# Kernel tuning notes

Measured on AMD Instinct MI355X. Metric: run time of the kernel, lower is better.

Reference implementation:

```python
import jax, jax.numpy as jnp
import numpy as np

B, S, D, H = 4, 2048, 1024, 16
DEPTH = D // H  # 64


def setup_inputs() -> dict:
    key = jax.random.key(0)
    ks = jax.random.split(key, 11)
    scale = 1.0 / np.sqrt(D)
    inp = {
        "v": jax.random.normal(ks[0], (B, S, D), jnp.float32),
        "k": jax.random.normal(ks[1], (B, S, D), jnp.float32),
        "q": jax.random.normal(ks[2], (B, S, D), jnp.float32),
        # causal mask: 1.0 where attention is disallowed (strict upper triangle)
        "mask": jnp.triu(jnp.ones((S, S), jnp.float32), k=1)[None, None, :, :],
        "wq": jax.random.normal(ks[3], (D, D), jnp.float32) * scale,
        "bq": jnp.zeros((D,), jnp.float32),
        "wk": jax.random.normal(ks[4], (D, D), jnp.float32) * scale,
        "bk": jnp.zeros((D,), jnp.float32),
        "wv": jax.random.normal(ks[5], (D, D), jnp.float32) * scale,
        "bv": jnp.zeros((D,), jnp.float32),
        "wo": jax.random.normal(ks[6], (D, D), jnp.float32) * scale,
        "bo": jnp.zeros((D,), jnp.float32),
    }
    return inp


def _split_heads(x):
    # [B, S, D] -> [B, H, S, depth]
    b, s, _ = x.shape
    return x.reshape(b, s, H, DEPTH).transpose(0, 2, 1, 3)


def reference(v, k, q, mask, wq, bq, wk, bk, wv, bv, wo, bo):
    qh = _split_heads(q @ wq + bq)  # [B,H,S,depth]
    kh = _split_heads(k @ wk + bk)
    vh = _split_heads(v @ wv + bv)

    logits = jnp.einsum("bhqd,bhkd->bhqk", qh, kh) / jnp.sqrt(
        jnp.asarray(DEPTH, jnp.float32)
    )
    logits = logits + mask * -1e9
    attn = jax.nn.softmax(logits, axis=-1)  # [B,H,S,S]
    out = jnp.einsum("bhqk,bhkd->bhqd", attn, vh)
    out = out.transpose(0, 2, 1, 3).reshape(q.shape[0], -1, D)  # [B,S,D]
    return out @ wo + bo
```

## Files before the change

### kernel.cpp

```cpp
#include <hip/hip_runtime.h>

typedef _Float16 f16;
typedef _Float16 half8 __attribute__((ext_vector_type(8)));
typedef _Float16 half4v __attribute__((ext_vector_type(4)));
typedef _Float16 half2v __attribute__((ext_vector_type(2)));
typedef float f32x4 __attribute__((ext_vector_type(4)));

__device__ __forceinline__ void gl_lds16(const void* g, void* l) {
    __builtin_amdgcn_global_load_lds((const __attribute__((address_space(1))) void*)g,
                                     (__attribute__((address_space(3))) void*)l, 16, 0, 0);
}

__device__ __forceinline__ unsigned pack_f16(float a, float b) {
    union { half2v h; unsigned u; } un;
    un.h[0] = (f16)a; un.h[1] = (f16)b;
    return un.u;
}

__global__ __launch_bounds__(256) void cvt_f32_f16(const float* __restrict__ x, f16* __restrict__ y)
{
    const size_t i = ((size_t)blockIdx.x * 256 + threadIdx.x) * 8;
    const float4 a = *(const float4*)(x + i);
    const float4 b = *(const float4*)(x + i + 4);
    half8 h;
    h[0] = (f16)a.x; h[1] = (f16)a.y; h[2] = (f16)a.z; h[3] = (f16)a.w;
    h[4] = (f16)b.x; h[5] = (f16)b.y; h[6] = (f16)b.z; h[7] = (f16)b.w;
    *(half8*)(y + i) = h;
}

__device__ __forceinline__ void prep_w_body(const float* __restrict__ W, f16* __restrict__ Wt)
{
    __shared__ float t[64][65];
    const int tid = threadIdx.x;
    const int tk = blockIdx.x * 64, tn = blockIdx.y * 64;
    const int rr = tid >> 4, cc = (tid & 15) * 4;
    #pragma unroll
    for (int j = 0; j < 4; ++j) {
        float4 v = *(const float4*)(W + (size_t)(tk + rr + j * 16) * 1024 + tn + cc);
        t[rr + j * 16][cc] = v.x; t[rr + j * 16][cc + 1] = v.y;
        t[rr + j * 16][cc + 2] = v.z; t[rr + j * 16][cc + 3] = v.w;
    }
    __syncthreads();
    const int n = tid >> 2, kc = (tid & 3) * 16;
    f16 o[16];
    #pragma unroll
    for (int j = 0; j < 16; ++j) o[j] = (f16)t[kc + j][n];
    f16* dst = Wt + (size_t)(tn + n) * 1024 + tk + kc;
    *(uint4*)dst = *(uint4*)o;
    *(uint4*)(dst + 8) = *(uint4*)(o + 8);
}

__global__ __launch_bounds__(256) void prep_w1(const float* __restrict__ W, f16* __restrict__ Wt)
{ prep_w_body(W, Wt); }

__global__ __launch_bounds__(256) void prep_w3(const float* __restrict__ w0,
    const float* __restrict__ w1, const float* __restrict__ w2, f16* __restrict__ Wt)
{
    const int z = blockIdx.z;
    const float* W = (z == 0) ? w0 : (z == 1) ? w1 : w2;
    prep_w_body(W, Wt + (size_t)z * 1024 * 1024);
}

template<int OUT>
__global__ __launch_bounds__(256, 2) void gemm_kernel(
    const f16* __restrict__ X, const f16* __restrict__ Wt,
    const float* __restrict__ bias, void* __restrict__ outv)
{
    __shared__ __align__(16) f16 As[2][128 * 64];
    __shared__ __align__(16) f16 Bs[2][128 * 64];

    const int tid = threadIdx.x;
    const int lane = tid & 63;
    const int lane16 = lane & 15, quad = lane >> 4;
    const int wave = tid >> 6;
    const int wm = (wave >> 1) * 64, wn = (wave & 1) * 64;

    const int lin = blockIdx.x + 8 * blockIdx.y;
    const int xcd = lin & 7, t = lin >> 3;
    const int m0 = ((t >> 3) * 8 + xcd) * 128;
    const int n0 = (t & 7) * 128;

    const int wbase = tid & 192;
    const int srow = tid >> 3, schunk = tid & 7;

    f32x4 acc[4][4] = {};

    #pragma unroll
    for (int i = 0; i < 4; ++i) {
        const int row = i * 32 + srow;
        const int sw = (schunk ^ (row & 7)) * 8;
        gl_lds16(Wt + (size_t)(n0 + row) * 1024 + sw, Bs[0] + (size_t)(i * 256 + wbase) * 8);
        gl_lds16(X  + (size_t)(m0 + row) * 1024 + sw, As[0] + (size_t)(i * 256 + wbase) * 8);
    }

    for (int kt = 0; kt < 16; ++kt) {
        if (kt + 1 < 16) {
            const int nb = (kt + 1) & 1;
            const int k1 = (kt + 1) * 64;
            #pragma unroll
            for (int i = 0; i < 4; ++i) {
                const int row = i * 32 + srow;
                const int sw = (schunk ^ (row & 7)) * 8;
                gl_lds16(Wt + (size_t)(n0 + row) * 1024 + k1 + sw, Bs[nb] + (size_t)(i * 256 + wbase) * 8);
                gl_lds16(X  + (size_t)(m0 + row) * 1024 + k1 + sw, As[nb] + (size_t)(i * 256 + wbase) * 8);
            }
            asm volatile("s_waitcnt vmcnt(8)" ::: "memory");
        } else {
            asm volatile("s_waitcnt vmcnt(0)" ::: "memory");
        }
        __builtin_amdgcn_s_barrier();
        asm volatile("" ::: "memory");

        const f16* Ab = As[kt & 1];
        const f16* Bb = Bs[kt & 1];
        half8 af[4][2], bf[4][2];
        #pragma unroll
        for (int i = 0; i < 4; ++i) {
            const int ra = wm + i * 16 + lane16;
            const int rb = wn + i * 16 + lane16;
            #pragma unroll
            for (int c = 0; c < 2; ++c) {
                af[i][c] = *(const half8*)(Ab + ra * 64 + (((c * 4 + quad) ^ (ra & 7)) * 8));
                bf[i][c] = *(const half8*)(Bb + rb * 64 + (((c * 4 + quad) ^ (rb & 7)) * 8));
            }
        }
        #pragma unroll
        for (int c = 0; c < 2; ++c)
            #pragma unroll
            for (int mi = 0; mi < 4; ++mi)
                #pragma unroll
                for (int ni = 0; ni < 4; ++ni)
                    acc[mi][ni] = __builtin_amdgcn_mfma_f32_16x16x32_f16(af[mi][c], bf[ni][c], acc[mi][ni], 0, 0, 0);

        asm volatile("" ::: "memory");
        __builtin_amdgcn_s_barrier();
        asm volatile("" ::: "memory");
    }

    #pragma unroll
    for (int mi = 0; mi < 4; ++mi) {
        #pragma unroll
        for (int ni = 0; ni < 4; ++ni) {
            const int col = n0 + wn + ni * 16 + lane16;
            const float bval = bias[col];
            const int grow0 = m0 + wm + mi * 16 + quad * 4;
            if (OUT == 2) {
                const int b = grow0 >> 11, s0 = grow0 & 2047;
                const int h = col >> 6, d = col & 63;
                half4v p;
                #pragma unroll
                for (int r = 0; r < 4; ++r) p[r] = (f16)(acc[mi][ni][r] + bval);
                *(half4v*)((f16*)outv + (((size_t)b * 16 + h) * 64 + d) * 2048 + s0) = p;
            } else if (OUT == 0) {
                #pragma unroll
                for (int r = 0; r < 4; ++r)
                    ((f16*)outv)[(size_t)(grow0 + r) * 1024 + col] = (f16)(acc[mi][ni][r] + bval);
            } else {
                #pragma unroll
                for (int r = 0; r < 4; ++r)
                    ((float*)outv)[(size_t)(grow0 + r) * 1024 + col] = acc[mi][ni][r] + bval;
            }
        }
    }
}

__global__ __launch_bounds__(256, 4) void attn_kernel(
    const f16* __restrict__ qh, const f16* __restrict__ kh,
    const f16* __restrict__ vt, f16* __restrict__ at)
{
    __shared__ __align__(16) f16 Ks[2][64 * 64];
    __shared__ __align__(16) f16 Vts[2][64 * 64];

    const int tid = threadIdx.x;
    const int lane = tid & 63, wave = tid >> 6;
    const int lane16 = lane & 15, quad = lane >> 4;
    const int wbase = tid & 192;
    const int l3 = lane16 & 7;
    const int srow = tid >> 3, schunk = tid & 7;

    const int lin = blockIdx.x + 16 * blockIdx.y;
    const int xcd = lin & 7, t = lin >> 3;
    const int bh = xcd + 8 * (t & 7);
    const int qi = 15 - (t >> 3);
    const int b = bh >> 4, h = bh & 15;

    const f16* qp = qh + (size_t)b * 2048 * 1024 + h * 64;
    const f16* kp = kh + (size_t)b * 2048 * 1024 + h * 64;
    const f16* vtp = vt + (size_t)bh * 64 * 2048;

    const int qb = 128 * qi;
    const int qrow0 = qb + wave * 32;
    const int ntiles = qb / 64 + 2;
    const int qmax = qrow0 + 31;

    #pragma unroll
    for (int i = 0; i < 2; ++i) {
        const int row = i * 32 + srow;
        const int sw = (schunk ^ (row & 7)) * 8;
        gl_lds16(kp + (size_t)row * 1024 + sw, Ks[0] + (size_t)(i * 256 + wbase) * 8);
        gl_lds16(vtp + (size_t)row * 2048 + sw, Vts[0] + (size_t)(i * 256 + wbase) * 8);
    }

    half8 aq[2][2];
    #pragma unroll
    for (int mt = 0; mt < 2; ++mt)
        #pragma unroll
        for (int c = 0; c < 2; ++c)
            aq[mt][c] = *(const half8*)(qp + (size_t)(qrow0 + mt * 16 + lane16) * 1024 + c * 32 + quad * 8);

    f32x4 o[4][2] = {};
    float lp[2] = {0.0f, 0.0f};

    for (int kt = 0; kt < ntiles; ++kt) {
        if (kt + 1 < ntiles) {
            const int nb = (kt + 1) & 1;
            const int k1 = (kt + 1) * 64;
            #pragma unroll
            for (int i = 0; i < 2; ++i) {
                const int row = i * 32 + srow;
                const int sw = (schunk ^ (row & 7)) * 8;
                gl_lds16(kp + (size_t)(k1 + row) * 1024 + sw, Ks[nb] + (size_t)(i * 256 + wbase) * 8);
                gl_lds16(vtp + (size_t)row * 2048 + k1 + sw, Vts[nb] + (size_t)(i * 256 + wbase) * 8);
            }
            asm volatile("s_waitcnt vmcnt(4)" ::: "memory");
        } else {
            asm volatile("s_waitcnt vmcnt(0)" ::: "memory");
        }
        __builtin_amdgcn_s_barrier();
        asm volatile("" ::: "memory");

        const int k0 = kt * 64;
        if (k0 <= qmax) {
            const f16* Kb = Ks[kt & 1];
            const f16* Vb = Vts[kt & 1];
            f32x4 sT[4][2];
            #pragma unroll
            for (int sub = 0; sub < 4; ++sub) {
                const int kr = sub * 16 + lane16;
                const half8 ak0 = *(const half8*)(Kb + kr * 64 + ((quad ^ l3) * 8));
                const half8 ak1 = *(const half8*)(Kb + kr * 64 + (((4 + quad) ^ l3) * 8));
                #pragma unroll
                for (int mt = 0; mt < 2; ++mt) {
                    f32x4 z = {};
                    z = __builtin_amdgcn_mfma_f32_16x16x32_f16(ak0, aq[mt][0], z, 0, 0, 0);
                    z = __builtin_amdgcn_mfma_f32_16x16x32_f16(ak1, aq[mt][1], z, 0, 0, 0);
                    sT[sub][mt] = z;
                }
            }
            const bool needmask = (k0 + 63 > qrow0);
            if (needmask) {
                #pragma unroll
                for (int sub = 0; sub < 4; ++sub)
                    #pragma unroll
                    for (int mt = 0; mt < 2; ++mt)
                        #pragma unroll
                        for (int r = 0; r < 4; ++r) {
                            const int key = k0 + sub * 16 + quad * 4 + r;
                            const int qi2 = qrow0 + mt * 16 + lane16;
                            if (key > qi2) sT[sub][mt][r] = -1e30f;
                        }
            }

            half8 bp[2][2];
            #pragma unroll
            for (int mt = 0; mt < 2; ++mt) {
                unsigned pk01[4], pk23[4];
                #pragma unroll
                for (int sub = 0; sub < 4; ++sub) {
                    float p[4];
                    #pragma unroll
                    for (int r = 0; r < 4; ++r) {
                        const float x = fmaf(sT[sub][mt][r], 0.18033688011112042f, -5.770780163555852f);
                        float e;
                        asm("v_exp_f32 %0, %1" : "=v"(e) : "v"(x));
                        p[r] = e;
                        lp[mt] += e;
                    }
                    pk01[sub] = pack_f16(p[0], p[1]);
                    pk23[sub] = pack_f16(p[2], p[3]);
                }
                #pragma unroll
                for (int c = 0; c < 2; ++c) {
                    unsigned a0 = pk01[2 * c], b0 = pk01[2 * c + 1];
                    unsigned a1 = pk23[2 * c], b1 = pk23[2 * c + 1];
                    asm("v_permlane32_swap_b32 %0, %1" : "+v"(a0), "+v"(b0));
                    asm("v_permlane16_swap_b32 %0, %1" : "+v"(a0), "+v"(b0));
                    asm("v_permlane32_swap_b32 %0, %1" : "+v"(a1), "+v"(b1));
                    asm("v_permlane16_swap_b32 %0, %1" : "+v"(a1), "+v"(b1));
                    union { unsigned u[4]; half8 h8; } un;
                    un.u[0] = a0; un.u[1] = a1; un.u[2] = b0; un.u[3] = b1;
                    bp[c][mt] = un.h8;
                }
            }

            #pragma unroll
            for (int nt = 0; nt < 4; ++nt) {
                const int dr = nt * 16 + lane16;
                const half8 av0 = *(const half8*)(Vb + dr * 64 + ((quad ^ l3) * 8));
                const half8 av1 = *(const half8*)(Vb + dr * 64 + (((4 + quad) ^ l3) * 8));
                #pragma unroll
                for (int mt = 0; mt < 2; ++mt) {
                    o[nt][mt] = __builtin_amdgcn_mfma_f32_16x16x32_f16(av0, bp[0][mt], o[nt][mt], 0, 0, 0);
                    o[nt][mt] = __builtin_amdgcn_mfma_f32_16x16x32_f16(av1, bp[1][mt], o[nt][mt], 0, 0, 0);
                }
            }
        }
        asm volatile("" ::: "memory");
        __builtin_amdgcn_s_barrier();
        asm volatile("" ::: "memory");
    }

    #pragma unroll
    for (int mt = 0; mt < 2; ++mt) {
        float red = lp[mt];
        red += __shfl_xor(red, 16);
        red += __shfl_xor(red, 32);
        const float inv = 1.0f / red;
        const int sr = qrow0 + mt * 16 + lane16;
        f16* dst = at + ((size_t)b * 2048 + sr) * 1024 + h * 64 + quad * 4;
        #pragma unroll
        for (int nt = 0; nt < 4; ++nt) {
            half4v p;
            #pragma unroll
            for (int r = 0; r < 4; ++r) p[r] = (f16)(o[nt][mt][r] * inv);
            *(half4v*)(dst + nt * 16) = p;
        }
    }
}

extern "C" void kernel_launch(void* const* d_in, const int* in_sizes, int n_in,
                              void* d_out, int out_size, void* d_ws, size_t ws_size,
                              hipStream_t stream)
{
    const float* v  = (const float*)d_in[0];
    const float* k  = (const float*)d_in[1];
    const float* q  = (const float*)d_in[2];
    const float* wq = (const float*)d_in[4];
    const float* bq = (const float*)d_in[5];
    const float* wk = (const float*)d_in[6];
    const float* bk = (const float*)d_in[7];
    const float* wv = (const float*)d_in[8];
    const float* bv = (const float*)d_in[9];
    const float* wo = (const float*)d_in[10];
    const float* bo = (const float*)d_in[11];

    f16* qh = (f16*)d_ws;
    f16* kh = qh + (size_t)8 * 1024 * 1024;
    f16* vt = kh + (size_t)8 * 1024 * 1024;
    f16* at = vt + (size_t)8 * 1024 * 1024;

    f16* wT = (f16*)d_out;
    f16* wqT = wT;
    f16* wkT = wT + (size_t)1024 * 1024;
    f16* wvT = wT + (size_t)2 * 1024 * 1024;
    f16* xf  = wT + (size_t)3 * 1024 * 1024;
    f16* woT = qh;

    prep_w3<<<dim3(16, 16, 3), 256, 0, stream>>>(wq, wk, wv, wT);

    dim3 g(8, 64);
    cvt_f32_f16<<<4096, 256, 0, stream>>>(q, xf);
    gemm_kernel<0><<<g, 256, 0, stream>>>(xf, wqT, bq, qh);
    cvt_f32_f16<<<4096, 256, 0, stream>>>(k, xf);
    gemm_kernel<0><<<g, 256, 0, stream>>>(xf, wkT, bk, kh);
    cvt_f32_f16<<<4096, 256, 0, stream>>>(v, xf);
    gemm_kernel<2><<<g, 256, 0, stream>>>(xf, wvT, bv, vt);

    attn_kernel<<<dim3(16, 64), 256, 0, stream>>>(qh, kh, vt, at);

    prep_w1<<<dim3(16, 16), 256, 0, stream>>>(wo, woT);
    gemm_kernel<1><<<g, 256, 0, stream>>>(at, woT, bo, d_out);
}
```

Measured before the change: 313.3 us.

## Fuse fp32-to-fp16 input conversion into a single batched QKV GEMM launch

Removes the three standalone fp32→fp16 conversion kernels. The QKV projection GEMM now loads fp32 activations straight into registers, converts them, and writes them to LDS during the pipelined K loop. The three projection GEMMs are also merged into one launch with a z-dimension of three, which cuts launch count and gives a larger grid. The cost is that A-tile loads go through registers instead of async global-to-LDS copies, which adds register pressure and a conversion step inside the main loop.

```diff
diff --git a/kernel.cpp b/kernel.cpp
--- a/kernel.cpp
+++ b/kernel.cpp
@@ -17,17 +17,6 @@
     return un.u;
 }
 
-__global__ __launch_bounds__(256) void cvt_f32_f16(const float* __restrict__ x, f16* __restrict__ y)
-{
-    const size_t i = ((size_t)blockIdx.x * 256 + threadIdx.x) * 8;
-    const float4 a = *(const float4*)(x + i);
-    const float4 b = *(const float4*)(x + i + 4);
-    half8 h;
-    h[0] = (f16)a.x; h[1] = (f16)a.y; h[2] = (f16)a.z; h[3] = (f16)a.w;
-    h[4] = (f16)b.x; h[5] = (f16)b.y; h[6] = (f16)b.z; h[7] = (f16)b.w;
-    *(half8*)(y + i) = h;
-}
-
 __device__ __forceinline__ void prep_w_body(const float* __restrict__ W, f16* __restrict__ Wt)
 {
     __shared__ float t[64][65];
@@ -61,13 +50,19 @@
     prep_w_body(W, Wt + (size_t)z * 1024 * 1024);
 }
 
-template<int OUT>
-__global__ __launch_bounds__(256, 2) void gemm_kernel(
-    const f16* __restrict__ X, const f16* __restrict__ Wt,
-    const float* __restrict__ bias, void* __restrict__ outv)
+__global__ __launch_bounds__(256, 2) void qkv_gemm(
+    const float* __restrict__ Xq, const float* __restrict__ Xk, const float* __restrict__ Xv,
+    const f16* __restrict__ Wt,
+    const float* __restrict__ bqp, const float* __restrict__ bkp, const float* __restrict__ bvp,
+    f16* __restrict__ qh, f16* __restrict__ kh, f16* __restrict__ vth)
 {
     __shared__ __align__(16) f16 As[2][128 * 64];
-    __shared__ __align__(16) f16 Bs[2][128 * 64];
+    __shared__ __align__(16) f16 Ws[2][128 * 64];
+
+    const int z = blockIdx.z;
+    const float* X    = (z == 0) ? Xq : (z == 1) ? Xk : Xv;
+    const float* bias = (z == 0) ? bqp : (z == 1) ? bkp : bvp;
+    const f16*   W    = Wt + (size_t)z * 1024 * 1024;
 
     const int tid = threadIdx.x;
     const int lane = tid & 63;
@@ -81,16 +76,150 @@
     const int n0 = (t & 7) * 128;
 
     const int wbase = tid & 192;
+    const int srow = tid >> 3;
+    const int sch  = tid & 7;
+    const int swc  = sch ^ (srow & 7);
+
+    const size_t xgbase = (size_t)(m0 + srow) * 1024 + sch * 8;
+    const size_t wgbase = (size_t)(n0 + srow) * 1024 + swc * 8;
+    f16* const pA0 = As[0] + srow * 64 + swc * 8;
+    f16* const pA1 = As[1] + srow * 64 + swc * 8;
+
+    f32x4 acc[4][4] = {};
+
+    {
+        float4 xr[4][2];
+        #pragma unroll
+        for (int i = 0; i < 4; ++i) {
+            xr[i][0] = *(const float4*)(X + xgbase + (size_t)i * 32768);
+            xr[i][1] = *(const float4*)(X + xgbase + (size_t)i * 32768 + 4);
+        }
+        #pragma unroll
+        for (int i = 0; i < 4; ++i)
+            gl_lds16(W + wgbase + (size_t)i * 32768, Ws[0] + (size_t)(i * 256 + wbase) * 8);
+        asm volatile("s_waitcnt vmcnt(4)" ::: "memory");
+        #pragma unroll
+        for (int i = 0; i < 4; ++i) {
+            half8 hx;
+            hx[0] = (f16)xr[i][0].x; hx[1] = (f16)xr[i][0].y;
+            hx[2] = (f16)xr[i][0].z; hx[3] = (f16)xr[i][0].w;
+            hx[4] = (f16)xr[i][1].x; hx[5] = (f16)xr[i][1].y;
+            hx[6] = (f16)xr[i][1].z; hx[7] = (f16)xr[i][1].w;
+            *(half8*)(pA0 + i * 2048) = hx;
+        }
+        asm volatile("s_waitcnt vmcnt(0) lgkmcnt(0)" ::: "memory");
+        __builtin_amdgcn_s_barrier();
+        asm volatile("" ::: "memory");
+    }
+
+    for (int kt = 0; kt < 16; ++kt) {
+        const int cur = kt & 1, nb = cur ^ 1;
+        float4 xr[4][2];
+        if (kt + 1 < 16) {
+            const int k1 = (kt + 1) * 64;
+            const float* xs = X + xgbase + k1;
+            #pragma unroll
+            for (int i = 0; i < 4; ++i) {
+                xr[i][0] = *(const float4*)(xs + (size_t)i * 32768);
+                xr[i][1] = *(const float4*)(xs + (size_t)i * 32768 + 4);
+            }
+            const f16* ws = W + wgbase + k1;
+            #pragma unroll
+            for (int i = 0; i < 4; ++i)
+                gl_lds16(ws + (size_t)i * 32768, Ws[nb] + (size_t)(i * 256 + wbase) * 8);
+        }
+
+        const f16* Ab = As[cur];
+        const f16* Bb = Ws[cur];
+        half8 af[4][2], bf[4][2];
+        #pragma unroll
+        for (int i = 0; i < 4; ++i) {
+            const int ra = wm + i * 16 + lane16;
+            const int rb = wn + i * 16 + lane16;
+            #pragma unroll
+            for (int c = 0; c < 2; ++c) {
+                af[i][c] = *(const half8*)(Ab + ra * 64 + (((c * 4 + quad) ^ (ra & 7)) * 8));
+                bf[i][c] = *(const half8*)(Bb + rb * 64 + (((c * 4 + quad) ^ (rb & 7)) * 8));
+            }
+        }
+        #pragma unroll
+        for (int c = 0; c < 2; ++c)
+            #pragma unroll
+            for (int mi = 0; mi < 4; ++mi)
+                #pragma unroll
+                for (int ni = 0; ni < 4; ++ni)
+                    acc[mi][ni] = __builtin_amdgcn_mfma_f32_16x16x32_f16(af[mi][c], bf[ni][c], acc[mi][ni], 0, 0, 0);
+
+        if (kt + 1 < 16) {
+            asm volatile("s_waitcnt vmcnt(4)" ::: "memory");
+            f16* pA = (nb == 0) ? pA0 : pA1;
+            #pragma unroll
+            for (int i = 0; i < 4; ++i) {
+                half8 hx;
+                hx[0] = (f16)xr[i][0].x; hx[1] = (f16)xr[i][0].y;
+                hx[2] = (f16)xr[i][0].z; hx[3] = (f16)xr[i][0].w;
+                hx[4] = (f16)xr[i][1].x; hx[5] = (f16)xr[i][1].y;
+                hx[6] = (f16)xr[i][1].z; hx[7] = (f16)xr[i][1].w;
+                *(half8*)(pA + i * 2048) = hx;
+            }
+        }
+        asm volatile("s_waitcnt vmcnt(0) lgkmcnt(0)" ::: "memory");
+        __builtin_amdgcn_s_barrier();
+        asm volatile("" ::: "memory");
+    }
+
+    #pragma unroll
+    for (int mi = 0; mi < 4; ++mi) {
+        #pragma unroll
+        for (int ni = 0; ni < 4; ++ni) {
+            const int col = n0 + wn + ni * 16 + lane16;
+            const float bval = bias[col];
+            const int grow0 = m0 + wm + mi * 16 + quad * 4;
+            if (z == 2) {
+                const int b = grow0 >> 11, s0 = grow0 & 2047;
+                const int h = col >> 6, d = col & 63;
+                half4v p;
+                #pragma unroll
+                for (int r = 0; r < 4; ++r) p[r] = (f16)(acc[mi][ni][r] + bval);
+                *(half4v*)(vth + (((size_t)b * 16 + h) * 64 + d) * 2048 + s0) = p;
+            } else {
+                f16* out = (z == 0) ? qh : kh;
+                #pragma unroll
+                for (int r = 0; r < 4; ++r)
+                    out[(size_t)(grow0 + r) * 1024 + col] = (f16)(acc[mi][ni][r] + bval);
+            }
+        }
+    }
+}
+
+__global__ __launch_bounds__(256, 2) void out_gemm(
+    const f16* __restrict__ X, const f16* __restrict__ Wt,
+    const float* __restrict__ bias, float* __restrict__ out)
+{
+    __shared__ __align__(16) f16 As[2][128 * 64];
+    __shared__ __align__(16) f16 Bs[2][128 * 64];
+
+    const int tid = threadIdx.x;
+    const int lane = tid & 63;
+    const int lane16 = lane & 15, quad = lane >> 4;
+    const int wave = tid >> 6;
+    const int wm = (wave >> 1) * 64, wn = (wave & 1) * 64;
+
+    const int lin = blockIdx.x + 8 * blockIdx.y;
+    const int xcd = lin & 7, t = lin >> 3;
+    const int m0 = ((t >> 3) * 8 + xcd) * 128;
+    const int n0 = (t & 7) * 128;
+
+    const int wbase = tid & 192;
     const int srow = tid >> 3, schunk = tid & 7;
+    const int swc = schunk ^ (srow & 7);
 
     f32x4 acc[4][4] = {};
 
     #pragma unroll
     for (int i = 0; i < 4; ++i) {
-        const int row = i * 32 + srow;
-        const int sw = (schunk ^ (row & 7)) * 8;
-        gl_lds16(Wt + (size_t)(n0 + row) * 1024 + sw, Bs[0] + (size_t)(i * 256 + wbase) * 8);
-        gl_lds16(X  + (size_t)(m0 + row) * 1024 + sw, As[0] + (size_t)(i * 256 + wbase) * 8);
+        gl_lds16(Wt + (size_t)(n0 + i * 32 + srow) * 1024 + swc * 8, Bs[0] + (size_t)(i * 256 + wbase) * 8);
+        gl_lds16(X  + (size_t)(m0 + i * 32 + srow) * 1024 + swc * 8, As[0] + (size_t)(i * 256 + wbase) * 8);
     }
 
     for (int kt = 0; kt < 16; ++kt) {
@@ -99,10 +228,8 @@
             const int k1 = (kt + 1) * 64;
             #pragma unroll
             for (int i = 0; i < 4; ++i) {
-                const int row = i * 32 + srow;
-                const int sw = (schunk ^ (row & 7)) * 8;
-                gl_lds16(Wt + (size_t)(n0 + row) * 1024 + k1 + sw, Bs[nb] + (size_t)(i * 256 + wbase) * 8);
-                gl_lds16(X  + (size_t)(m0 + row) * 1024 + k1 + sw, As[nb] + (size_t)(i * 256 + wbase) * 8);
+                gl_lds16(Wt + (size_t)(n0 + i * 32 + srow) * 1024 + k1 + swc * 8, Bs[nb] + (size_t)(i * 256 + wbase) * 8);
+                gl_lds16(X  + (size_t)(m0 + i * 32 + srow) * 1024 + k1 + swc * 8, As[nb] + (size_t)(i * 256 + wbase) * 8);
             }
             asm volatile("s_waitcnt vmcnt(8)" ::: "memory");
         } else {
@@ -144,22 +271,9 @@
             const int col = n0 + wn + ni * 16 + lane16;
             const float bval = bias[col];
             const int grow0 = m0 + wm + mi * 16 + quad * 4;
-            if (OUT == 2) {
-                const int b = grow0 >> 11, s0 = grow0 & 2047;
-                const int h = col >> 6, d = col & 63;
-                half4v p;
-                #pragma unroll
-                for (int r = 0; r < 4; ++r) p[r] = (f16)(acc[mi][ni][r] + bval);
-                *(half4v*)((f16*)outv + (((size_t)b * 16 + h) * 64 + d) * 2048 + s0) = p;
-            } else if (OUT == 0) {
-                #pragma unroll
-                for (int r = 0; r < 4; ++r)
-                    ((f16*)outv)[(size_t)(grow0 + r) * 1024 + col] = (f16)(acc[mi][ni][r] + bval);
-            } else {
-                #pragma unroll
-                for (int r = 0; r < 4; ++r)
-                    ((float*)outv)[(size_t)(grow0 + r) * 1024 + col] = acc[mi][ni][r] + bval;
-            }
+            #pragma unroll
+            for (int r = 0; r < 4; ++r)
+                out[(size_t)(grow0 + r) * 1024 + col] = acc[mi][ni][r] + bval;
         }
     }
 }
@@ -350,24 +464,14 @@
     f16* at = vt + (size_t)8 * 1024 * 1024;
 
     f16* wT = (f16*)d_out;
-    f16* wqT = wT;
-    f16* wkT = wT + (size_t)1024 * 1024;
-    f16* wvT = wT + (size_t)2 * 1024 * 1024;
-    f16* xf  = wT + (size_t)3 * 1024 * 1024;
     f16* woT = qh;
 
     prep_w3<<<dim3(16, 16, 3), 256, 0, stream>>>(wq, wk, wv, wT);
 
-    dim3 g(8, 64);
-    cvt_f32_f16<<<4096, 256, 0, stream>>>(q, xf);
-    gemm_kernel<0><<<g, 256, 0, stream>>>(xf, wqT, bq, qh);
-    cvt_f32_f16<<<4096, 256, 0, stream>>>(k, xf);
-    gemm_kernel<0><<<g, 256, 0, stream>>>(xf, wkT, bk, kh);
-    cvt_f32_f16<<<4096, 256, 0, stream>>>(v, xf);
-    gemm_kernel<2><<<g, 256, 0, stream>>>(xf, wvT, bv, vt);
+    qkv_gemm<<<dim3(8, 64, 3), 256, 0, stream>>>(q, k, v, wT, bq, bk, bv, qh, kh, vt);
 
     attn_kernel<<<dim3(16, 64), 256, 0, stream>>>(qh, kh, vt, at);
 
     prep_w1<<<dim3(16, 16), 256, 0, stream>>>(wo, woT);
-    gemm_kernel<1><<<g, 256, 0, stream>>>(at, woT, bo, d_out);
-}
+    out_gemm<<<dim3(8, 64), 256, 0, stream>>>(at, woT, bo, (float*)d_out);
+}
```

Measured after the change: 330.7 us. 1.06x slower.
